# Kernel optimization log

Hardware: AMD Instinct MI355X
Metric: run time of the kernel (lower is better)

The kernel has to match this reference:

```python
import jax, jax.numpy as jnp
import numpy as np


def reference(x, y, max_disp):
    # x, y: [B, C, H, W] left/right feature maps (stride-3 features)
    # Builds cost[b, :C, i, h, w]  = x[b, :, h, w]      for w >= i else 0
    #        cost[b, C:, i, h, w] = y[b, :, h, w - i]  for w >= i else 0
    # i.e. the vectorized form of the original Python loop over disparities.
    D = max_disp // 3
    B, C, H, W = x.shape
    d = jnp.arange(D)
    w = jnp.arange(W)
    mask = (w[None, :] >= d[:, None]).astype(x.dtype)          # [D, W]
    m = mask[None, None, :, None, :]                            # [1,1,D,1,W]
    cost_x = x[:, :, None, :, :] * m                            # [B,C,D,H,W]
    idx = jnp.clip(w[None, :] - d[:, None], 0, W - 1)           # [D, W]
    y_shift = y[:, :, :, idx]                                   # [B,C,H,D,W]
    cost_y = jnp.transpose(y_shift, (0, 1, 3, 2, 4)) * m        # [B,C,D,H,W]
    return jnp.concatenate([cost_x, cost_y], axis=1)            # [B,2C,D,H,W]


def setup_inputs() -> dict:
    key = jax.random.key(0)
    k1, k2 = jax.random.split(key)
    B, C, H, W = 1, 32, 96, 192
    x = jax.random.normal(k1, (B, C, H, W), dtype=jnp.float32)
    y = jax.random.normal(k2, (B, C, H, W), dtype=jnp.float32)
    return {"x": x, "y": y, "max_disp": 192}
```

## Files before the change

### kernel.cpp

```cpp
#include <hip/hip_runtime.h>

constexpr int C      = 32;
constexpr int D      = 64;
constexpr int H      = 96;
constexpr int W      = 192;
constexpr int W4     = W / 4;
constexpr int DCHUNK = 16;
constexpr int NCHUNK = D / DCHUNK;

typedef float f4 __attribute__((ext_vector_type(4)));

__global__ __launch_bounds__(256) void fusion_kernel(const float* __restrict__ x,
                                                     const float* __restrict__ y,
                                                     float* __restrict__ out) {
    const int tid  = blockIdx.x * blockDim.x + threadIdx.x;
    const int w4   = tid % W4;
    int rest       = tid / W4;
    const int h    = rest % H;
    rest          /= H;
    const int ch   = rest % (2 * C);
    const int d0   = (rest / (2 * C)) * DCHUNK;
    const int w    = w4 * 4;

    int outoff = (ch * D + d0) * (H * W) + h * W + w;

    if (ch < C) {
        const f4 xv = *(const f4*)(&x[(ch * H + h) * W + w]);
        #pragma unroll
        for (int i = 0; i < DCHUNK; ++i) {
            const int d = d0 + i;
            f4 v = xv;
            if (w < d) {
                if (w + 0 < d) v.x = 0.f;
                if (w + 1 < d) v.y = 0.f;
                if (w + 2 < d) v.z = 0.f;
                if (w + 3 < d) v.w = 0.f;
            }
            *(f4*)(&out[outoff + i * (H * W)]) = v;
        }
    } else {
        const float* yr = &y[((ch - C) * H + h) * W];
        f4 v;
        v.x = yr[max(w + 0 - d0, 0)];
        v.y = yr[max(w + 1 - d0, 0)];
        v.z = yr[max(w + 2 - d0, 0)];
        v.w = yr[max(w + 3 - d0, 0)];
        #pragma unroll
        for (int i = 0; i < DCHUNK; ++i) {
            const int d = d0 + i;
            f4 s = v;
            if (w < d) {
                if (w + 0 < d) s.x = 0.f;
                if (w + 1 < d) s.y = 0.f;
                if (w + 2 < d) s.z = 0.f;
                if (w + 3 < d) s.w = 0.f;
            }
            *(f4*)(&out[outoff + i * (H * W)]) = s;
            v.w = v.z; v.z = v.y; v.y = v.x;
            v.x = yr[max(w - d - 1, 0)];
        }
    }
}

extern "C" void kernel_launch(void* const* d_in, const int* in_sizes, int n_in,
                              void* d_out, int out_size, void* d_ws, size_t ws_size,
                              hipStream_t stream) {
    const float* x = (const float*)d_in[0];
    const float* y = (const float*)d_in[1];
    float* out     = (float*)d_out;

    constexpr int total  = 2 * C * H * W4 * NCHUNK;
    constexpr int block  = 256;
    constexpr int grid   = total / block;
    fusion_kernel<<<grid, block, 0, stream>>>(x, y, out);
}
```

Measured before the change: 306.1 us.

## Use grid-stride loop with one float4 output per iteration and unaligned y loads

Replaces the per-thread disparity chunk loop with a grid-stride loop over the flattened output. Each iteration writes one float4, so consecutive threads write contiguous memory. Each y element is now read with one unaligned vector load instead of a shift-register of scalar loads. The goal is fully coalesced streaming stores and a fixed grid size. In exchange, source reads are repeated per disparity plane instead of reused in registers, and each element needs index divisions.

```diff
diff --git a/kernel.cpp b/kernel.cpp
--- a/kernel.cpp
+++ b/kernel.cpp
@@ -4,61 +4,46 @@
 constexpr int D      = 64;
 constexpr int H      = 96;
 constexpr int W      = 192;
-constexpr int W4     = W / 4;
-constexpr int DCHUNK = 16;
-constexpr int NCHUNK = D / DCHUNK;
+constexpr int PLANE4 = H * W / 4;
+constexpr int TOTAL4 = 2 * C * D * PLANE4;
 
-typedef float f4 __attribute__((ext_vector_type(4)));
+typedef float f4  __attribute__((ext_vector_type(4)));
+typedef float f4u __attribute__((ext_vector_type(4), aligned(4)));
 
 __global__ __launch_bounds__(256) void fusion_kernel(const float* __restrict__ x,
                                                      const float* __restrict__ y,
                                                      float* __restrict__ out) {
-    const int tid  = blockIdx.x * blockDim.x + threadIdx.x;
-    const int w4   = tid % W4;
-    int rest       = tid / W4;
-    const int h    = rest % H;
-    rest          /= H;
-    const int ch   = rest % (2 * C);
-    const int d0   = (rest / (2 * C)) * DCHUNK;
-    const int w    = w4 * 4;
+    const int nthreads = gridDim.x * blockDim.x;
+    int o4 = blockIdx.x * blockDim.x + threadIdx.x;
+    #pragma unroll 2
+    for (; o4 < TOTAL4; o4 += nthreads) {
+        const int chd = o4 / PLANE4;
+        const int rem = o4 - chd * PLANE4;
+        const int ch  = chd >> 6;
+        const int d   = chd & 63;
+        const int w   = (rem % 48) * 4;
 
-    int outoff = (ch * D + d0) * (H * W) + h * W + w;
-
-    if (ch < C) {
-        const f4 xv = *(const f4*)(&x[(ch * H + h) * W + w]);
-        #pragma unroll
-        for (int i = 0; i < DCHUNK; ++i) {
-            const int d = d0 + i;
-            f4 v = xv;
-            if (w < d) {
-                if (w + 0 < d) v.x = 0.f;
-                if (w + 1 < d) v.y = 0.f;
-                if (w + 2 < d) v.z = 0.f;
-                if (w + 3 < d) v.w = 0.f;
+        f4 v;
+        if (ch < C) {
+            v = *(const f4*)(x + ch * (H * W) + rem * 4);
+        } else {
+            const int off = (ch - C) * (H * W) + rem * 4 - d;
+            if (off >= 0) {
+                v = *(const f4u*)(y + off);
+            } else {
+                v.x = y[max(off + 0, 0)];
+                v.y = y[max(off + 1, 0)];
+                v.z = y[max(off + 2, 0)];
+                v.w = y[max(off + 3, 0)];
             }
-            *(f4*)(&out[outoff + i * (H * W)]) = v;
         }
-    } else {
-        const float* yr = &y[((ch - C) * H + h) * W];
-        f4 v;
-        v.x = yr[max(w + 0 - d0, 0)];
-        v.y = yr[max(w + 1 - d0, 0)];
-        v.z = yr[max(w + 2 - d0, 0)];
-        v.w = yr[max(w + 3 - d0, 0)];
-        #pragma unroll
-        for (int i = 0; i < DCHUNK; ++i) {
-            const int d = d0 + i;
-            f4 s = v;
-            if (w < d) {
-                if (w + 0 < d) s.x = 0.f;
-                if (w + 1 < d) s.y = 0.f;
-                if (w + 2 < d) s.z = 0.f;
-                if (w + 3 < d) s.w = 0.f;
-            }
-            *(f4*)(&out[outoff + i * (H * W)]) = s;
-            v.w = v.z; v.z = v.y; v.y = v.x;
-            v.x = yr[max(w - d - 1, 0)];
+        if (w < d) {
+            if (w + 0 < d) v.x = 0.f;
+            if (w + 1 < d) v.y = 0.f;
+            if (w + 2 < d) v.z = 0.f;
+            if (w + 3 < d) v.w = 0.f;
         }
+        *(f4*)(out + (long long)o4 * 4) = v;
     }
 }
 
@@ -69,8 +54,7 @@
     const float* y = (const float*)d_in[1];
     float* out     = (float*)d_out;
 
-    constexpr int total  = 2 * C * H * W4 * NCHUNK;
-    constexpr int block  = 256;
-    constexpr int grid   = total / block;
+    constexpr int block = 256;
+    constexpr int grid  = 4608;
     fusion_kernel<<<grid, block, 0, stream>>>(x, y, out);
 }
```

New measurement: 322.1 us. 1.05x slower.
